# Kernel tuning notes

Measured on AMD Instinct MI355X. Metric: run time of the kernel, lower is better.

## Reference

```python
import jax, jax.numpy as jnp
import numpy as np

NUM_LAYERS, NUM_HEADS, DH, C = 5, 4, 32, 128
B, T, HH, WW = 2, 12, 32, 32


def conv2d(x, w, b):
    # x: (N, Cin, H, W), w: (Cout, Cin, 3, 3) same padding
    y = jax.lax.conv_general_dilated(x, w, window_strides=(1, 1), padding='SAME',
                                     dimension_numbers=('NCHW', 'OIHW', 'NCHW'))
    return y + b[None, :, None, None]


def sine_pos(length, depth):
    pos = jnp.arange(length, dtype=jnp.float32)[:, None]
    div = jnp.exp(jnp.arange(0, depth, 2, dtype=jnp.float32) * (-np.log(10000.0) / depth))
    pe = jnp.zeros((length, depth), dtype=jnp.float32)
    pe = pe.at[:, 0::2].set(jnp.sin(pos * div))
    pe = pe.at[:, 1::2].set(jnp.cos(pos * div))
    return pe[None, :, :, None, None]  # (1, L, dh, 1, 1) broadcasts over batch & spatial


def group_norm(x, scale, bias, groups=4, eps=1e-5):
    n, c, h, w = x.shape
    xg = x.reshape(n, groups, c // groups, h, w)
    mu = xg.mean(axis=(2, 3, 4), keepdims=True)
    var = ((xg - mu) ** 2).mean(axis=(2, 3, 4), keepdims=True)
    xg = (xg - mu) * jax.lax.rsqrt(var + eps)
    return xg.reshape(n, c, h, w) * scale[None, :, None, None] + bias[None, :, None, None]


def head_forward(x, pos, qw, qb, kvw, kvb, aw, ab):
    # x: (B, L, dh, H, W)
    b, l, c, h, w = x.shape
    xf = x.reshape(b * l, c, h, w)
    q = conv2d(xf, qw, qb).reshape(b, l, c, h, w) + pos
    v = conv2d(xf, kvw, kvb).reshape(b, l, c, h, w)  # k and v share features
    k = v + pos
    # pairwise concat: (B, Lq, Lk, 2*dh, H, W)
    qe = jnp.broadcast_to(q[:, :, None], (b, l, l, c, h, w))
    ke = jnp.broadcast_to(k[:, None, :], (b, l, l, c, h, w))
    qk = jnp.concatenate([qe, ke], axis=3).reshape(b * l * l, 2 * c, h, w)
    att = conv2d(qk, aw, ab).reshape(b, l, l, 1, h, w)
    att = jax.nn.softmax(att, axis=2)  # softmax over key-frame axis
    return jnp.sum(att * v[:, None], axis=2)  # (B, L, dh, H, W)


def reference(input_tensor, q_w, q_b, kv_w, kv_b, att_w, att_b,
              ff1_w, ff1_b, ff2_w, ff2_b, gn_w, gn_b):
    num_layers, num_heads = q_w.shape[0], q_w.shape[1]
    b, l, c, h, w = input_tensor.shape
    dh = c // num_heads
    pos = sine_pos(l, dh)
    out = input_tensor
    for li in range(num_layers):
        heads = [head_forward(out[:, :, i * dh:(i + 1) * dh], pos,
                              q_w[li, i], q_b[li, i], kv_w[li, i], kv_b[li, i],
                              att_w[li, i], att_b[li, i])
                 for i in range(num_heads)]
        att_out = jnp.concatenate(heads, axis=2) + out  # residual
        att_flat = att_out.reshape(b * l, c, h, w)
        ff = conv2d(jax.nn.relu(conv2d(att_flat, ff1_w[li], ff1_b[li])), ff2_w[li], ff2_b[li])
        y = group_norm(ff + att_flat, gn_w[li], gn_b[li])
        out = y.reshape(b, l, c, h, w)
    return out


def setup_inputs() -> dict:
    key = jax.random.key(0)
    ks = jax.random.split(key, 12)
    f = lambda k, s, sc=1.0: jax.random.normal(k, s, dtype=jnp.float32) * sc
    L, H = NUM_LAYERS, NUM_HEADS
    return {
        'input_tensor': f(ks[0], (B, T, C, HH, WW)),
        'q_w': f(ks[1], (L, H, DH, DH, 3, 3), 0.05),
        'q_b': f(ks[2], (L, H, DH), 0.05),
        'kv_w': f(ks[3], (L, H, DH, DH, 3, 3), 0.05),
        'kv_b': f(ks[4], (L, H, DH), 0.05),
        'att_w': f(ks[5], (L, H, 1, 2 * DH, 3, 3), 0.05),
        'att_b': f(ks[6], (L, H, 1), 0.05),
        'ff1_w': f(ks[7], (L, C, C, 3, 3), 0.03),
        'ff1_b': f(ks[8], (L, C), 0.03),
        'ff2_w': f(ks[9], (L, C, C, 3, 3), 0.03),
        'ff2_b': f(ks[10], (L, C), 0.03),
        'gn_w': jnp.ones((L, C), dtype=jnp.float32),
        'gn_b': jnp.zeros((L, C), dtype=jnp.float32),
    }
```

## Files before the change

### kernel.cpp

```cpp
#include <hip/hip_runtime.h>

#define NELEM 3145728
#define IMG 24
#define CH 128
#define HW 1024
#define PADP 1156
#define A2IMG 147968

using short8   = __attribute__((ext_vector_type(8))) short;
using float4v  = __attribute__((ext_vector_type(4))) float;
using float16v = __attribute__((ext_vector_type(16))) float;

__device__ inline unsigned short f2bf(float f){
    union { float f; unsigned u; } c; c.f = f;
    return (unsigned short)((c.u + 0x7FFF + ((c.u >> 16) & 1)) >> 16);
}
__device__ inline float bf2f(unsigned short h){
    union { unsigned u; float f; } c; c.u = ((unsigned)h) << 16; return c.f;
}

__global__ __launch_bounds__(256) void k_prep(
    const float* __restrict__ ff1w, const float* __restrict__ ff2w,
    const float* __restrict__ kvw, const float* __restrict__ input,
    unsigned short* __restrict__ Wd, unsigned short* __restrict__ Wkv,
    unsigned short* __restrict__ A2a, unsigned short* __restrict__ A2v,
    float* __restrict__ cur)
{
    int gid = blockIdx.x * 256 + threadIdx.x;
    if (gid < 1474560) {
        int idx = gid;
        int li2 = idx / 147456, r1 = idx - li2 * 147456;
        int j = r1 & 7, co = (r1 >> 3) & 127;
        int kh = (r1 >> 10) & 1, k16 = (r1 >> 11) & 7, tap = r1 >> 14;
        int ci = k16 * 16 + kh * 8 + j;
        const float* base = ((li2 & 1) ? ff2w : ff1w) + (size_t)(li2 >> 1) * 147456;
        Wd[idx] = f2bf(base[(co * 128 + ci) * 9 + tap]);
    } else if (gid < 1658880) {
        int idx = gid - 1474560;
        int li = idx / 36864, r1 = idx - li * 36864;
        int j = r1 & 7, co = (r1 >> 3) & 127;
        int kh = (r1 >> 10) & 1, k16 = (r1 >> 11) & 1, tap = r1 >> 12;
        int h = co >> 5, colc = co & 31, cil = k16 * 16 + kh * 8 + j;
        Wkv[idx] = f2bf(kvw[((size_t)((li * 4 + h) * 32 + colc) * 32 + cil) * 9 + tap]);
    } else if (gid < 2469888) {
        int g2 = gid - 1658880;
        int c = g2 & 127, r = g2 >> 7;
        int bp = r % 132, r2 = r / 132;
        int img = r2 % 24, buf = r2 / 24;
        int pos;
        if (bp < 34) pos = bp;
        else if (bp < 68) pos = 33 * 34 + (bp - 34);
        else if (bp < 100) pos = (bp - 68 + 1) * 34;
        else pos = (bp - 100 + 1) * 34 + 33;
        unsigned short* p = buf ? A2v : A2a;
        p[(size_t)img * A2IMG + pos * 128 + c] = 0;
    } else {
        int g2 = gid - 2469888;
        int c4 = (g2 & 31) * 4, px = (g2 >> 5) & 1023, img = g2 >> 15;
        float4v v;
        #pragma unroll
        for (int j = 0; j < 4; j++)
            v[j] = input[((size_t)img * 128 + c4 + j) * HW + px];
        *(float4v*)(cur + ((size_t)img * HW + px) * 128 + c4) = v;
        int pos = ((px >> 5) + 1) * 34 + (px & 31) + 1;
        unsigned short* ap = A2a + ((size_t)img * PADP + pos) * 128 + c4;
        #pragma unroll
        for (int j = 0; j < 4; j++) ap[j] = f2bf(v[j]);
    }
}

template<bool GROUPED, bool RELU, bool RES, bool EF32, bool EA2, bool STAT>
__global__ __launch_bounds__(256, 3) void k_conv(
    const unsigned short* __restrict__ a2in, const unsigned short* __restrict__ w2,
    const float* __restrict__ bias, const float* __restrict__ res,
    float* __restrict__ outf, unsigned short* __restrict__ outa2,
    float* __restrict__ pstat)
{
    const int y = blockIdx.x;
    const int img = blockIdx.y;
    const int t = threadIdx.x;
    const int wave = t >> 6, lane = t & 63;
    const int col = lane & 31, kh = lane >> 5;
    const int cog = wave * 32;
    const int head = wave;

    constexpr int NK16 = GROUPED ? 2 : 8;

    __shared__ unsigned short sA[102 * 136];

    const unsigned short* slab = a2in + (size_t)img * A2IMG + (size_t)y * 34 * 128;
    #pragma unroll
    for (int it = 0; it < 7; it++) {
        int u = it * 256 + t;
        if (u < 1632) {
            int px = u >> 4, g = u & 15;
            short8 vv = *reinterpret_cast<const short8*>(slab + px * 128 + g * 8);
            *reinterpret_cast<short8*>(sA + px * 136 + g * 8) = vv;
        }
    }

    const short8* w8 = reinterpret_cast<const short8*>(w2);
    const int bl = kh * 128 + cog + col;

    short8 bfr[2][NK16];
    auto loadB = [&](int tap, int buf){
        #pragma unroll
        for (int k16 = 0; k16 < NK16; k16++)
            bfr[buf][k16] = w8[(tap * NK16 + k16) * 256 + bl];
    };
    loadB(0, 0);

    float16v acc;
    #pragma unroll
    for (int r = 0; r < 16; r++) acc[r] = 0.f;

    __syncthreads();

    const int cibase = (GROUPED ? head * 32 : 0) + kh * 8;
    #pragma unroll
    for (int tap = 0; tap < 9; tap++) {
        if (tap + 1 < 9) loadB(tap + 1, (tap + 1) & 1);
        const int ky = tap / 3, kx = tap - ky * 3;
        const int pxl = ky * 34 + kx + col;
        #pragma unroll
        for (int k16 = 0; k16 < NK16; k16++) {
            short8 a = *reinterpret_cast<const short8*>(
                sA + pxl * 136 + cibase + k16 * 16);
            acc = __builtin_amdgcn_mfma_f32_32x32x16_bf16(
                a, bfr[tap & 1][k16], acc, 0, 0, 0);
        }
    }

    float s1 = 0.f, s2 = 0.f;
    const int co = cog + col;
    const float bb = bias[co];
    #pragma unroll
    for (int r = 0; r < 16; r++) {
        int pxr = (r & 3) + 8 * (r >> 2) + 4 * kh;
        int px = y * 32 + pxr;
        float val = acc[r] + bb;
        if (RELU) val = fmaxf(val, 0.f);
        size_t ci = ((size_t)img * HW + px) * 128 + co;
        if (RES) val += res[ci];
        if (EF32) outf[ci] = val;
        if (EA2) {
            int pos = (y + 1) * 34 + pxr + 1;
            outa2[((size_t)img * PADP + pos) * 128 + co] = f2bf(val);
        }
        if (STAT) { s1 += val; s2 += val * val; }
    }
    if (STAT) {
        #pragma unroll
        for (int o = 32; o > 0; o >>= 1) {
            s1 += __shfl_down(s1, o); s2 += __shfl_down(s2, o);
        }
        if (lane == 0) {
            atomicAdd(&pstat[(img * 4 + head) * 2], s1);
            atomicAdd(&pstat[(img * 4 + head) * 2 + 1], s2);
        }
    }
}

__global__ __launch_bounds__(256) void k_attn(
    const unsigned short* __restrict__ a2v, const float* __restrict__ aw,
    float* __restrict__ ak, float* __restrict__ pstat)
{
    const int img = blockIdx.x;
    const int h = blockIdx.y;
    const int y0 = blockIdx.z * 8;
    const int t = threadIdx.x;
    const int b = img / 12, l = img - b * 12;

    if (blockIdx.x == 0 && blockIdx.y == 0 && blockIdx.z == 0 && t < 192)
        pstat[t] = 0.f;

    __shared__ float sxv[32 * 341];
    __shared__ float spos[32];
    if (t < 32) {
        int j2 = t & ~1;
        float freq = __expf(-(float)j2 * 0.28782313662425576f);
        float ang = (float)l * freq;
        spos[t] = (t & 1) ? __cosf(ang) : __sinf(ang);
    }
    __syncthreads();

    const unsigned short* vb = a2v + (size_t)img * A2IMG + h * 32;
    for (int idx = t; idx < 1360; idx += 256) {
        int q = idx & 3, pos = idx >> 2;
        int ppos = y0 * 34 + pos;
        int row = y0 + pos / 34, col = pos - (pos / 34) * 34;
        bool inter = (row >= 1 && row <= 32 && col >= 1 && col <= 32);
        short8 vv = *reinterpret_cast<const short8*>(vb + (size_t)ppos * 128 + q * 8);
        #pragma unroll
        for (int j = 0; j < 8; j++) {
            float f = bf2f((unsigned short)vv[j]);
            if (inter) f += spos[q * 8 + j];
            sxv[(q * 8 + j) * 341 + pos] = f;
        }
    }
    __syncthreads();

    const float* wb = aw + (h * 64 + 32) * 9;
    const int r = t >> 5, xx = t & 31;
    float acc = 0.f;
    #pragma unroll 4
    for (int ci = 0; ci < 32; ci++) {
        #pragma unroll
        for (int ky = 0; ky < 3; ky++)
            #pragma unroll
            for (int kx = 0; kx < 3; kx++)
                acc = fmaf(sxv[ci * 341 + (r + ky) * 34 + xx + kx],
                           wb[ci * 9 + ky * 3 + kx], acc);
    }
    ak[((b * 4 + h) * 12 + l) * HW + (y0 + r) * 32 + xx] = acc;
}

__global__ __launch_bounds__(256) void k_wsum(const float* __restrict__ ak,
    const float* __restrict__ v, float* __restrict__ cur,
    unsigned short* __restrict__ a2a)
{
    int gid = blockIdx.x * 256 + threadIdx.x;
    int c4 = (gid & 31) * 4, px = (gid >> 5) & 1023, b = gid >> 15;
    int h = c4 >> 5;
    const float* wp = ak + ((b * 4 + h) * 12) * HW + px;
    float a[12], m = -1e30f;
    #pragma unroll
    for (int l = 0; l < 12; l++) { a[l] = wp[l * HW]; m = fmaxf(m, a[l]); }
    float ssum = 0.f;
    #pragma unroll
    for (int l = 0; l < 12; l++) { a[l] = __expf(a[l] - m); ssum += a[l]; }
    float invs = 1.f / ssum;
    float4v s = (float4v){0.f,0.f,0.f,0.f};
    #pragma unroll
    for (int l = 0; l < 12; l++) {
        float4v vv = *(const float4v*)(v + (((size_t)(b * 12 + l) * HW) + px) * 128 + c4);
        #pragma unroll
        for (int j = 0; j < 4; j++) s[j] += a[l] * vv[j];
    }
    #pragma unroll
    for (int j = 0; j < 4; j++) s[j] *= invs;
    int pos = ((px >> 5) + 1) * 34 + (px & 31) + 1;
    #pragma unroll
    for (int l = 0; l < 12; l++) {
        size_t ci = (((size_t)(b * 12 + l) * HW) + px) * 128 + c4;
        float4v cv = *(float4v*)(cur + ci);
        #pragma unroll
        for (int j = 0; j < 4; j++) cv[j] += s[j];
        *(float4v*)(cur + ci) = cv;
        unsigned short* ap = a2a + ((size_t)(b * 12 + l) * PADP + pos) * 128 + c4;
        #pragma unroll
        for (int j = 0; j < 4; j++) ap[j] = f2bf(cv[j]);
    }
}

template<bool LAST>
__global__ __launch_bounds__(256) void k_gnapply(const float* __restrict__ y,
    const float* __restrict__ pstat, const float* __restrict__ gw,
    const float* __restrict__ gb, float* __restrict__ cur,
    unsigned short* __restrict__ a2a, float* __restrict__ outp)
{
    int gid = blockIdx.x * 256 + threadIdx.x;
    if (!LAST) {
        int c4 = (gid & 31) * 4, px = (gid >> 5) & 1023, img = gid >> 15;
        int g = c4 >> 5;
        float S = pstat[(img * 4 + g) * 2], Q = pstat[(img * 4 + g) * 2 + 1];
        float mu = S * (1.f / 32768.f);
        float inv = rsqrtf(Q * (1.f / 32768.f) - mu * mu + 1e-5f);
        float4v vv = *(const float4v*)(y + ((size_t)img * HW + px) * 128 + c4);
        int pos = ((px >> 5) + 1) * 34 + (px & 31) + 1;
        size_t ci = ((size_t)img * HW + px) * 128 + c4;
        unsigned short* ap = a2a + ((size_t)img * PADP + pos) * 128 + c4;
        #pragma unroll
        for (int j = 0; j < 4; j++) {
            float val = (vv[j] - mu) * inv * gw[c4 + j] + gb[c4 + j];
            vv[j] = val;
            ap[j] = f2bf(val);
        }
        *(float4v*)(cur + ci) = vv;
    } else {
        int px4 = (gid & 255) * 4, c = (gid >> 8) & 127, img = gid >> 15;
        int g = c >> 5;
        float S = pstat[(img * 4 + g) * 2], Q = pstat[(img * 4 + g) * 2 + 1];
        float mu = S * (1.f / 32768.f);
        float inv = rsqrtf(Q * (1.f / 32768.f) - mu * mu + 1e-5f);
        float gg = gw[c], bb = gb[c];
        float4v o;
        #pragma unroll
        for (int j = 0; j < 4; j++) {
            float val = y[((size_t)img * HW + px4 + j) * 128 + c];
            o[j] = (val - mu) * inv * gg + bb;
        }
        *(float4v*)(outp + ((size_t)img * 128 + c) * HW + px4) = o;
    }
}

extern "C" void kernel_launch(void* const* d_in, const int* in_sizes, int n_in,
                              void* d_out, int out_size, void* d_ws, size_t ws_size,
                              hipStream_t stream)
{
    const float* input = (const float*)d_in[0];
    const float* kv_w  = (const float*)d_in[3];
    const float* kv_b  = (const float*)d_in[4];
    const float* att_w = (const float*)d_in[5];
    const float* ff1_w = (const float*)d_in[7];
    const float* ff1_b = (const float*)d_in[8];
    const float* ff2_w = (const float*)d_in[9];
    const float* ff2_b = (const float*)d_in[10];
    const float* gn_w  = (const float*)d_in[11];
    const float* gn_b  = (const float*)d_in[12];

    float* ws  = (float*)d_ws;
    float* cur = ws;
    float* ak  = ws + (size_t)NELEM;
    float* pstat = ak + 98304;
    unsigned short* W2d  = (unsigned short*)(pstat + 192);
    unsigned short* W2kv = W2d + 1474560;
    unsigned short* A2v  = W2kv + 184320;
    unsigned short* A2a  = A2v + (size_t)IMG * A2IMG;
    float* v    = (float*)d_out;
    float* outp = (float*)d_out;

    k_prep<<<12720, 256, 0, stream>>>(ff1_w, ff2_w, kv_w, input,
                                      W2d, W2kv, A2a, A2v, cur);

    for (int li = 0; li < 5; li++) {
        k_conv<true, false, false, true, true, false><<<dim3(32, IMG), 256, 0, stream>>>(
            A2a, W2kv + (size_t)li * 36864, kv_b + li * 128, nullptr, v, A2v, nullptr);
        k_attn<<<dim3(IMG, 4, 4), 256, 0, stream>>>(A2v, att_w + (size_t)li * 2304, ak, pstat);
        k_wsum<<<256, 256, 0, stream>>>(ak, v, cur, A2a);
        k_conv<false, true, false, false, true, false><<<dim3(32, IMG), 256, 0, stream>>>(
            A2a, W2d + (size_t)(li * 2 + 0) * 147456, ff1_b + li * 128, nullptr, nullptr, A2v, nullptr);
        k_conv<false, false, true, true, false, true><<<dim3(32, IMG), 256, 0, stream>>>(
            A2v, W2d + (size_t)(li * 2 + 1) * 147456, ff2_b + li * 128, cur, cur, nullptr, pstat);
        if (li == 4)
            k_gnapply<true><<<3072, 256, 0, stream>>>(cur, pstat, gn_w + li * 128,
                gn_b + li * 128, nullptr, nullptr, outp);
        else
            k_gnapply<false><<<3072, 256, 0, stream>>>(cur, pstat, gn_w + li * 128,
                gn_b + li * 128, cur, A2a, nullptr);
    }
}
```

Baseline: 518.1 us.

## Fuse kv conv into attention kernel and defer group norm into next layer

The grouped kv convolution now runs inside the attention-logit kernel. Each block recomputes a 10-row halo of v from fp32 cur via MFMA, so the v bf16 padded buffer no longer needs a round trip through global memory. Group-norm application is deferred: the next layer's kvattn and wsum kernels normalize cur on the fly, using ping-ponged statistics buffers. That removes the per-layer gnapply launch and the A2a staging buffer. The ff1 conv converts fp32 cur to bf16 while loading its tile. The cost is redundant halo-row conv work, extra per-element normalization arithmetic, and more shared memory in the fused kernel.

```diff
diff --git a/kernel.cpp b/kernel.cpp
--- a/kernel.cpp
+++ b/kernel.cpp
@@ -8,23 +8,20 @@
 #define A2IMG 147968
 
 using short8   = __attribute__((ext_vector_type(8))) short;
+using ushort4v = __attribute__((ext_vector_type(4))) unsigned short;
 using float4v  = __attribute__((ext_vector_type(4))) float;
 using float16v = __attribute__((ext_vector_type(16))) float;
 
 __device__ inline unsigned short f2bf(float f){
     union { float f; unsigned u; } c; c.f = f;
     return (unsigned short)((c.u + 0x7FFF + ((c.u >> 16) & 1)) >> 16);
-}
-__device__ inline float bf2f(unsigned short h){
-    union { unsigned u; float f; } c; c.u = ((unsigned)h) << 16; return c.f;
 }
 
 __global__ __launch_bounds__(256) void k_prep(
     const float* __restrict__ ff1w, const float* __restrict__ ff2w,
     const float* __restrict__ kvw, const float* __restrict__ input,
     unsigned short* __restrict__ Wd, unsigned short* __restrict__ Wkv,
-    unsigned short* __restrict__ A2a, unsigned short* __restrict__ A2v,
-    float* __restrict__ cur)
+    unsigned short* __restrict__ A2v, float* __restrict__ cur)
 {
     int gid = blockIdx.x * 256 + threadIdx.x;
     if (gid < 1474560) {
@@ -42,71 +39,184 @@
         int kh = (r1 >> 10) & 1, k16 = (r1 >> 11) & 1, tap = r1 >> 12;
         int h = co >> 5, colc = co & 31, cil = k16 * 16 + kh * 8 + j;
         Wkv[idx] = f2bf(kvw[((size_t)((li * 4 + h) * 32 + colc) * 32 + cil) * 9 + tap]);
-    } else if (gid < 2469888) {
+    } else if (gid < 2064384) {
         int g2 = gid - 1658880;
         int c = g2 & 127, r = g2 >> 7;
-        int bp = r % 132, r2 = r / 132;
-        int img = r2 % 24, buf = r2 / 24;
+        int bp = r % 132, img = r / 132;
         int pos;
         if (bp < 34) pos = bp;
         else if (bp < 68) pos = 33 * 34 + (bp - 34);
         else if (bp < 100) pos = (bp - 68 + 1) * 34;
         else pos = (bp - 100 + 1) * 34 + 33;
-        unsigned short* p = buf ? A2v : A2a;
-        p[(size_t)img * A2IMG + pos * 128 + c] = 0;
+        A2v[(size_t)img * A2IMG + pos * 128 + c] = 0;
     } else {
-        int g2 = gid - 2469888;
+        int g2 = gid - 2064384;
         int c4 = (g2 & 31) * 4, px = (g2 >> 5) & 1023, img = g2 >> 15;
         float4v v;
         #pragma unroll
         for (int j = 0; j < 4; j++)
             v[j] = input[((size_t)img * 128 + c4 + j) * HW + px];
         *(float4v*)(cur + ((size_t)img * HW + px) * 128 + c4) = v;
-        int pos = ((px >> 5) + 1) * 34 + (px & 31) + 1;
-        unsigned short* ap = A2a + ((size_t)img * PADP + pos) * 128 + c4;
-        #pragma unroll
-        for (int j = 0; j < 4; j++) ap[j] = f2bf(v[j]);
-    }
-}
-
-template<bool GROUPED, bool RELU, bool RES, bool EF32, bool EA2, bool STAT>
+    }
+}
+
+__global__ __launch_bounds__(256, 2) void k_kvattn(
+    const float* __restrict__ cur, const unsigned short* __restrict__ wkv,
+    const float* __restrict__ kvb, const float* __restrict__ aw,
+    const float* __restrict__ pstatp, const float* __restrict__ gw,
+    const float* __restrict__ gb, float* __restrict__ v,
+    float* __restrict__ ak, float* __restrict__ pstatz)
+{
+    const int img = blockIdx.x, h = blockIdx.y, y0 = blockIdx.z * 8;
+    const int t = threadIdx.x;
+    const int b = img / 12, l = img - b * 12;
+
+    if (blockIdx.x == 0 && blockIdx.y == 0 && blockIdx.z == 0 && t < 192)
+        pstatz[t] = 0.f;
+
+    __shared__ float sxv[32 * 341];
+    __shared__ unsigned short slab[408 * 40];
+    __shared__ float spos[32], sbias[32], sgw[32], sgb[32];
+
+    if (t < 32) {
+        int j2 = t & ~1;
+        float freq = __expf(-(float)j2 * 0.28782313662425576f);
+        float ang = (float)l * freq;
+        spos[t] = (t & 1) ? __cosf(ang) : __sinf(ang);
+        sbias[t] = kvb[h * 32 + t];
+        sgw[t] = gw ? gw[h * 32 + t] : 1.f;
+        sgb[t] = gb ? gb[h * 32 + t] : 0.f;
+    }
+    float mu = 0.f, inv = 1.f;
+    if (pstatp) {
+        float S = pstatp[(img * 4 + h) * 2], Q = pstatp[(img * 4 + h) * 2 + 1];
+        mu = S * (1.f / 32768.f);
+        inv = rsqrtf(Q * (1.f / 32768.f) - mu * mu + 1e-5f);
+    }
+    __syncthreads();
+
+    for (int u = t; u < 3264; u += 256) {
+        int q = u & 7, p = u >> 3;
+        int lr = p / 34, lc = p - lr * 34;
+        int yr = y0 - 2 + lr, x = lc - 1;
+        float4v val = (float4v){0.f, 0.f, 0.f, 0.f};
+        if (yr >= 0 && yr < 32 && x >= 0 && x < 32) {
+            val = *(const float4v*)(cur + ((size_t)img * HW + yr * 32 + x) * 128 + h * 32 + q * 4);
+            #pragma unroll
+            for (int j = 0; j < 4; j++)
+                val[j] = (val[j] - mu) * inv * sgw[q * 4 + j] + sgb[q * 4 + j];
+        }
+        ushort4v o;
+        #pragma unroll
+        for (int j = 0; j < 4; j++) o[j] = f2bf(val[j]);
+        *(ushort4v*)(slab + p * 40 + q * 4) = o;
+    }
+    __syncthreads();
+
+    const int lane = t & 63, wave = t >> 6;
+    const int colx = lane & 31, kh = lane >> 5;
+    const short8* w8 = reinterpret_cast<const short8*>(wkv);
+
+    for (int f = wave; f < 10; f += 4) {
+        float16v acc;
+        #pragma unroll
+        for (int r = 0; r < 16; r++) acc[r] = 0.f;
+        #pragma unroll
+        for (int tap = 0; tap < 9; tap++) {
+            const int ky = tap / 3, kx = tap - ky * 3;
+            #pragma unroll
+            for (int k16 = 0; k16 < 2; k16++) {
+                short8 a = *reinterpret_cast<const short8*>(
+                    slab + ((f + ky) * 34 + colx + kx) * 40 + k16 * 16 + kh * 8);
+                short8 bf = w8[((tap * 2 + k16) * 2 + kh) * 128 + h * 32 + colx];
+                acc = __builtin_amdgcn_mfma_f32_32x32x16_bf16(a, bf, acc, 0, 0, 0);
+            }
+        }
+        const int yr = y0 - 1 + f;
+        const bool rowin = (yr >= 0 && yr < 32);
+        const bool vown = rowin && f >= 1 && f <= 8;
+        const float posci = spos[colx], bb = sbias[colx];
+        float* vrow = v + ((size_t)img * HW + yr * 32) * 128 + h * 32 + colx;
+        #pragma unroll
+        for (int r = 0; r < 16; r++) {
+            int x2 = (r & 3) + 8 * (r >> 2) + 4 * kh;
+            float val = rowin ? acc[r] + bb : 0.f;
+            if (vown) vrow[(size_t)x2 * 128] = val;
+            sxv[colx * 341 + f * 34 + x2 + 1] = rowin ? val + posci : 0.f;
+        }
+    }
+    for (int u = t; u < 640; u += 256) {
+        int ci = u & 31, r2 = u >> 5;
+        sxv[ci * 341 + (r2 >> 1) * 34 + ((r2 & 1) ? 33 : 0)] = 0.f;
+    }
+    __syncthreads();
+
+    const float* wb = aw + (h * 64 + 32) * 9;
+    const int r = t >> 5, xx = t & 31;
+    float acc2 = 0.f;
+    #pragma unroll 4
+    for (int ci = 0; ci < 32; ci++) {
+        #pragma unroll
+        for (int ky = 0; ky < 3; ky++)
+            #pragma unroll
+            for (int kx = 0; kx < 3; kx++)
+                acc2 = fmaf(sxv[ci * 341 + (r + ky) * 34 + xx + kx],
+                            wb[ci * 9 + ky * 3 + kx], acc2);
+    }
+    ak[((size_t)(b * 4 + h) * 12 + l) * HW + (y0 + r) * 32 + xx] = acc2;
+}
+
+template<bool SRC32, bool RELU, bool RES, bool EF32, bool EA2, bool STAT>
 __global__ __launch_bounds__(256, 3) void k_conv(
-    const unsigned short* __restrict__ a2in, const unsigned short* __restrict__ w2,
-    const float* __restrict__ bias, const float* __restrict__ res,
-    float* __restrict__ outf, unsigned short* __restrict__ outa2,
-    float* __restrict__ pstat)
+    const unsigned short* __restrict__ a2in, const float* __restrict__ src32,
+    const unsigned short* __restrict__ w2, const float* __restrict__ bias,
+    const float* __restrict__ res, float* __restrict__ outf,
+    unsigned short* __restrict__ outa2, float* __restrict__ pstat)
 {
     const int y = blockIdx.x;
     const int img = blockIdx.y;
     const int t = threadIdx.x;
     const int wave = t >> 6, lane = t & 63;
-    const int col = lane & 31, kh = lane >> 5;
+    const int colx = lane & 31, kh = lane >> 5;
     const int cog = wave * 32;
     const int head = wave;
 
-    constexpr int NK16 = GROUPED ? 2 : 8;
-
     __shared__ unsigned short sA[102 * 136];
 
-    const unsigned short* slab = a2in + (size_t)img * A2IMG + (size_t)y * 34 * 128;
-    #pragma unroll
-    for (int it = 0; it < 7; it++) {
-        int u = it * 256 + t;
-        if (u < 1632) {
-            int px = u >> 4, g = u & 15;
-            short8 vv = *reinterpret_cast<const short8*>(slab + px * 128 + g * 8);
-            *reinterpret_cast<short8*>(sA + px * 136 + g * 8) = vv;
+    if (SRC32) {
+        for (int u = t; u < 3264; u += 256) {
+            int q = u & 31, p = u >> 5;
+            int lr = p / 34, lc = p - lr * 34;
+            int yr = y - 1 + lr, x = lc - 1;
+            float4v val = (float4v){0.f, 0.f, 0.f, 0.f};
+            if (yr >= 0 && yr < 32 && x >= 0 && x < 32)
+                val = *(const float4v*)(src32 + ((size_t)img * HW + yr * 32 + x) * 128 + q * 4);
+            ushort4v o;
+            #pragma unroll
+            for (int j = 0; j < 4; j++) o[j] = f2bf(val[j]);
+            *(ushort4v*)(sA + p * 136 + q * 4) = o;
+        }
+    } else {
+        const unsigned short* slab = a2in + (size_t)img * A2IMG + (size_t)y * 34 * 128;
+        #pragma unroll
+        for (int it = 0; it < 7; it++) {
+            int u = it * 256 + t;
+            if (u < 1632) {
+                int px = u >> 4, g = u & 15;
+                short8 vv = *reinterpret_cast<const short8*>(slab + px * 128 + g * 8);
+                *reinterpret_cast<short8*>(sA + px * 136 + g * 8) = vv;
+            }
         }
     }
 
     const short8* w8 = reinterpret_cast<const short8*>(w2);
-    const int bl = kh * 128 + cog + col;
-
-    short8 bfr[2][NK16];
+    const int bl = kh * 128 + cog + colx;
+
+    short8 bfr[2][8];
     auto loadB = [&](int tap, int buf){
         #pragma unroll
-        for (int k16 = 0; k16 < NK16; k16++)
-            bfr[buf][k16] = w8[(tap * NK16 + k16) * 256 + bl];
+        for (int k16 = 0; k16 < 8; k16++)
+            bfr[buf][k16] = w8[(tap * 8 + k16) * 256 + bl];
     };
     loadB(0, 0);
 
@@ -116,14 +226,14 @@
 
     __syncthreads();
 
-    const int cibase = (GROUPED ? head * 32 : 0) + kh * 8;
+    const int cibase = kh * 8;
     #pragma unroll
     for (int tap = 0; tap < 9; tap++) {
         if (tap + 1 < 9) loadB(tap + 1, (tap + 1) & 1);
         const int ky = tap / 3, kx = tap - ky * 3;
-        const int pxl = ky * 34 + kx + col;
-        #pragma unroll
-        for (int k16 = 0; k16 < NK16; k16++) {
+        const int pxl = ky * 34 + kx + colx;
+        #pragma unroll
+        for (int k16 = 0; k16 < 8; k16++) {
             short8 a = *reinterpret_cast<const short8*>(
                 sA + pxl * 136 + cibase + k16 * 16);
             acc = __builtin_amdgcn_mfma_f32_32x32x16_bf16(
@@ -132,7 +242,7 @@
     }
 
     float s1 = 0.f, s2 = 0.f;
-    const int co = cog + col;
+    const int co = cog + colx;
     const float bb = bias[co];
     #pragma unroll
     for (int r = 0; r < 16; r++) {
@@ -161,63 +271,10 @@
     }
 }
 
-__global__ __launch_bounds__(256) void k_attn(
-    const unsigned short* __restrict__ a2v, const float* __restrict__ aw,
-    float* __restrict__ ak, float* __restrict__ pstat)
-{
-    const int img = blockIdx.x;
-    const int h = blockIdx.y;
-    const int y0 = blockIdx.z * 8;
-    const int t = threadIdx.x;
-    const int b = img / 12, l = img - b * 12;
-
-    if (blockIdx.x == 0 && blockIdx.y == 0 && blockIdx.z == 0 && t < 192)
-        pstat[t] = 0.f;
-
-    __shared__ float sxv[32 * 341];
-    __shared__ float spos[32];
-    if (t < 32) {
-        int j2 = t & ~1;
-        float freq = __expf(-(float)j2 * 0.28782313662425576f);
-        float ang = (float)l * freq;
-        spos[t] = (t & 1) ? __cosf(ang) : __sinf(ang);
-    }
-    __syncthreads();
-
-    const unsigned short* vb = a2v + (size_t)img * A2IMG + h * 32;
-    for (int idx = t; idx < 1360; idx += 256) {
-        int q = idx & 3, pos = idx >> 2;
-        int ppos = y0 * 34 + pos;
-        int row = y0 + pos / 34, col = pos - (pos / 34) * 34;
-        bool inter = (row >= 1 && row <= 32 && col >= 1 && col <= 32);
-        short8 vv = *reinterpret_cast<const short8*>(vb + (size_t)ppos * 128 + q * 8);
-        #pragma unroll
-        for (int j = 0; j < 8; j++) {
-            float f = bf2f((unsigned short)vv[j]);
-            if (inter) f += spos[q * 8 + j];
-            sxv[(q * 8 + j) * 341 + pos] = f;
-        }
-    }
-    __syncthreads();
-
-    const float* wb = aw + (h * 64 + 32) * 9;
-    const int r = t >> 5, xx = t & 31;
-    float acc = 0.f;
-    #pragma unroll 4
-    for (int ci = 0; ci < 32; ci++) {
-        #pragma unroll
-        for (int ky = 0; ky < 3; ky++)
-            #pragma unroll
-            for (int kx = 0; kx < 3; kx++)
-                acc = fmaf(sxv[ci * 341 + (r + ky) * 34 + xx + kx],
-                           wb[ci * 9 + ky * 3 + kx], acc);
-    }
-    ak[((b * 4 + h) * 12 + l) * HW + (y0 + r) * 32 + xx] = acc;
-}
-
 __global__ __launch_bounds__(256) void k_wsum(const float* __restrict__ ak,
     const float* __restrict__ v, float* __restrict__ cur,
-    unsigned short* __restrict__ a2a)
+    const float* __restrict__ pstatp, const float* __restrict__ gw,
+    const float* __restrict__ gb)
 {
     int gid = blockIdx.x * 256 + threadIdx.x;
     int c4 = (gid & 31) * 4, px = (gid >> 5) & 1023, b = gid >> 15;
@@ -230,7 +287,7 @@
     #pragma unroll
     for (int l = 0; l < 12; l++) { a[l] = __expf(a[l] - m); ssum += a[l]; }
     float invs = 1.f / ssum;
-    float4v s = (float4v){0.f,0.f,0.f,0.f};
+    float4v s = (float4v){0.f, 0.f, 0.f, 0.f};
     #pragma unroll
     for (int l = 0; l < 12; l++) {
         float4v vv = *(const float4v*)(v + (((size_t)(b * 12 + l) * HW) + px) * 128 + c4);
@@ -239,59 +296,48 @@
     }
     #pragma unroll
     for (int j = 0; j < 4; j++) s[j] *= invs;
-    int pos = ((px >> 5) + 1) * 34 + (px & 31) + 1;
+    float gwv[4], gbv[4];
+    #pragma unroll
+    for (int j = 0; j < 4; j++) {
+        gwv[j] = gw ? gw[c4 + j] : 1.f;
+        gbv[j] = gb ? gb[c4 + j] : 0.f;
+    }
     #pragma unroll
     for (int l = 0; l < 12; l++) {
-        size_t ci = (((size_t)(b * 12 + l) * HW) + px) * 128 + c4;
+        int img = b * 12 + l;
+        float mu = 0.f, inv = 1.f;
+        if (pstatp) {
+            float S = pstatp[(img * 4 + h) * 2], Q = pstatp[(img * 4 + h) * 2 + 1];
+            mu = S * (1.f / 32768.f);
+            inv = rsqrtf(Q * (1.f / 32768.f) - mu * mu + 1e-5f);
+        }
+        size_t ci = (((size_t)img * HW) + px) * 128 + c4;
         float4v cv = *(float4v*)(cur + ci);
         #pragma unroll
-        for (int j = 0; j < 4; j++) cv[j] += s[j];
+        for (int j = 0; j < 4; j++)
+            cv[j] = (cv[j] - mu) * inv * gwv[j] + gbv[j] + s[j];
         *(float4v*)(cur + ci) = cv;
-        unsigned short* ap = a2a + ((size_t)(b * 12 + l) * PADP + pos) * 128 + c4;
-        #pragma unroll
-        for (int j = 0; j < 4; j++) ap[j] = f2bf(cv[j]);
-    }
-}
-
-template<bool LAST>
-__global__ __launch_bounds__(256) void k_gnapply(const float* __restrict__ y,
+    }
+}
+
+__global__ __launch_bounds__(256) void k_gnlast(const float* __restrict__ y,
     const float* __restrict__ pstat, const float* __restrict__ gw,
-    const float* __restrict__ gb, float* __restrict__ cur,
-    unsigned short* __restrict__ a2a, float* __restrict__ outp)
+    const float* __restrict__ gb, float* __restrict__ outp)
 {
     int gid = blockIdx.x * 256 + threadIdx.x;
-    if (!LAST) {
-        int c4 = (gid & 31) * 4, px = (gid >> 5) & 1023, img = gid >> 15;
-        int g = c4 >> 5;
-        float S = pstat[(img * 4 + g) * 2], Q = pstat[(img * 4 + g) * 2 + 1];
-        float mu = S * (1.f / 32768.f);
-        float inv = rsqrtf(Q * (1.f / 32768.f) - mu * mu + 1e-5f);
-        float4v vv = *(const float4v*)(y + ((size_t)img * HW + px) * 128 + c4);
-        int pos = ((px >> 5) + 1) * 34 + (px & 31) + 1;
-        size_t ci = ((size_t)img * HW + px) * 128 + c4;
-        unsigned short* ap = a2a + ((size_t)img * PADP + pos) * 128 + c4;
-        #pragma unroll
-        for (int j = 0; j < 4; j++) {
-            float val = (vv[j] - mu) * inv * gw[c4 + j] + gb[c4 + j];
-            vv[j] = val;
-            ap[j] = f2bf(val);
-        }
-        *(float4v*)(cur + ci) = vv;
-    } else {
-        int px4 = (gid & 255) * 4, c = (gid >> 8) & 127, img = gid >> 15;
-        int g = c >> 5;
-        float S = pstat[(img * 4 + g) * 2], Q = pstat[(img * 4 + g) * 2 + 1];
-        float mu = S * (1.f / 32768.f);
-        float inv = rsqrtf(Q * (1.f / 32768.f) - mu * mu + 1e-5f);
-        float gg = gw[c], bb = gb[c];
-        float4v o;
-        #pragma unroll
-        for (int j = 0; j < 4; j++) {
-            float val = y[((size_t)img * HW + px4 + j) * 128 + c];
-            o[j] = (val - mu) * inv * gg + bb;
-        }
-        *(float4v*)(outp + ((size_t)img * 128 + c) * HW + px4) = o;
-    }
+    int px4 = (gid & 255) * 4, c = (gid >> 8) & 127, img = gid >> 15;
+    int g = c >> 5;
+    float S = pstat[(img * 4 + g) * 2], Q = pstat[(img * 4 + g) * 2 + 1];
+    float mu = S * (1.f / 32768.f);
+    float inv = rsqrtf(Q * (1.f / 32768.f) - mu * mu + 1e-5f);
+    float gg = gw[c], bb = gb[c];
+    float4v o;
+    #pragma unroll
+    for (int j = 0; j < 4; j++) {
+        float val = y[((size_t)img * HW + px4 + j) * 128 + c];
+        o[j] = (val - mu) * inv * gg + bb;
+    }
+    *(float4v*)(outp + ((size_t)img * 128 + c) * HW + px4) = o;
 }
 
 extern "C" void kernel_launch(void* const* d_in, const int* in_sizes, int n_in,
@@ -313,30 +359,31 @@
     float* cur = ws;
     float* ak  = ws + (size_t)NELEM;
     float* pstat = ak + 98304;
-    unsigned short* W2d  = (unsigned short*)(pstat + 192);
+    unsigned short* W2d  = (unsigned short*)(pstat + 384);
     unsigned short* W2kv = W2d + 1474560;
     unsigned short* A2v  = W2kv + 184320;
-    unsigned short* A2a  = A2v + (size_t)IMG * A2IMG;
     float* v    = (float*)d_out;
     float* outp = (float*)d_out;
 
-    k_prep<<<12720, 256, 0, stream>>>(ff1_w, ff2_w, kv_w, input,
-                                      W2d, W2kv, A2a, A2v, cur);
+    k_prep<<<11136, 256, 0, stream>>>(ff1_w, ff2_w, kv_w, input, W2d, W2kv, A2v, cur);
 
     for (int li = 0; li < 5; li++) {
-        k_conv<true, false, false, true, true, false><<<dim3(32, IMG), 256, 0, stream>>>(
-            A2a, W2kv + (size_t)li * 36864, kv_b + li * 128, nullptr, v, A2v, nullptr);
-        k_attn<<<dim3(IMG, 4, 4), 256, 0, stream>>>(A2v, att_w + (size_t)li * 2304, ak, pstat);
-        k_wsum<<<256, 256, 0, stream>>>(ak, v, cur, A2a);
-        k_conv<false, true, false, false, true, false><<<dim3(32, IMG), 256, 0, stream>>>(
-            A2a, W2d + (size_t)(li * 2 + 0) * 147456, ff1_b + li * 128, nullptr, nullptr, A2v, nullptr);
+        float* psC = pstat + (li & 1) * 192;
+        const float* psP = li ? pstat + ((li - 1) & 1) * 192 : nullptr;
+        const float* gwP = li ? gn_w + (li - 1) * 128 : nullptr;
+        const float* gbP = li ? gn_b + (li - 1) * 128 : nullptr;
+
+        k_kvattn<<<dim3(IMG, 4, 4), 256, 0, stream>>>(
+            cur, W2kv + (size_t)li * 36864, kv_b + li * 128, att_w + (size_t)li * 2304,
+            psP, gwP, gbP, v, ak, psC);
+        k_wsum<<<256, 256, 0, stream>>>(ak, v, cur, psP, gwP, gbP);
+        k_conv<true, true, false, false, true, false><<<dim3(32, IMG), 256, 0, stream>>>(
+            nullptr, cur, W2d + (size_t)(li * 2 + 0) * 147456, ff1_b + li * 128,
+            nullptr, nullptr, A2v, nullptr);
         k_conv<false, false, true, true, false, true><<<dim3(32, IMG), 256, 0, stream>>>(
-            A2v, W2d + (size_t)(li * 2 + 1) * 147456, ff2_b + li * 128, cur, cur, nullptr, pstat);
-        if (li == 4)
-            k_gnapply<true><<<3072, 256, 0, stream>>>(cur, pstat, gn_w + li * 128,
-                gn_b + li * 128, nullptr, nullptr, outp);
-        else
-            k_gnapply<false><<<3072, 256, 0, stream>>>(cur, pstat, gn_w + li * 128,
-                gn_b + li * 128, cur, A2a, nullptr);
-    }
-}
+            A2v, nullptr, W2d + (size_t)(li * 2 + 1) * 147456, ff2_b + li * 128,
+            cur, cur, nullptr, psC);
+    }
+    k_gnlast<<<3072, 256, 0, stream>>>(cur, pstat + 0, gn_w + 4 * 128,
+                                       gn_b + 4 * 128, outp);
+}
```

Result: faster. 507.4 us (-2.0%).
